# Optimization experiments

Measured on AMD Instinct MI355X. Metric: run time of the kernel, lower is better.

## Reference

```python
import jax, jax.numpy as jnp
import numpy as np

DIM = 64   # flow dimension
HID = 8    # hidden_dim=[8]
B = 131072 # batch of samples


def setup_inputs() -> dict:
    key = jax.random.key(0)
    ks = jax.random.split(key, 6)
    L = DIM - 1  # number of per-dim MLPs (layers[0..L-1], layer l has fan-in l+1)
    lim = float(np.sqrt(0.5))
    x = jax.random.normal(ks[0], (B, DIM), jnp.float32)
    initial_param = jax.random.uniform(ks[1], (2,), jnp.float32, -lim, lim)
    # Ragged Linear(fan_in=l+1, 8) weights stacked into padded [L, HID, L];
    # entries beyond column l are masked to zero in reference().
    fan_in = np.arange(1, DIM).astype(np.float32)          # (L,)
    bnd1 = (1.0 / np.sqrt(fan_in))[:, None, None]          # torch Linear default init bound
    W1 = jax.random.uniform(ks[2], (L, HID, L), jnp.float32, -1.0, 1.0) * bnd1
    b1 = jax.random.uniform(ks[3], (L, HID), jnp.float32, -1.0, 1.0) * bnd1[:, :, 0]
    bnd2 = 1.0 / np.sqrt(HID)
    W2 = jax.random.uniform(ks[4], (L, 2, HID), jnp.float32, -bnd2, bnd2)
    b2 = jax.random.uniform(ks[5], (L, 2), jnp.float32, -bnd2, bnd2)
    return {"x": x, "initial_param": initial_param, "W1": W1, "b1": b1, "W2": W2, "b2": b2}


def reference(x, initial_param, W1, b1, W2, b2):
    B_, D = x.shape
    L = W1.shape[0]  # D - 1
    # mask[l, d] = 1 iff d <= l  ->  layer l sees exactly x[:, :l+1]
    mask = jnp.tril(jnp.ones((L, L), x.dtype))
    W1m = W1 * mask[:, None, :]
    # all dim-1 tiny MLPs fused into two batched contractions
    h = jnp.tanh(jnp.einsum('bd,lhd->blh', x[:, :L], W1m) + b1)   # [B, L, HID]
    out = jnp.einsum('blh,loh->blo', h, W2) + b2                   # [B, L, 2]
    mu0 = jnp.broadcast_to(initial_param[0], (B_, 1)).astype(x.dtype)
    al0 = jnp.broadcast_to(initial_param[1], (B_, 1)).astype(x.dtype)
    mu = jnp.concatenate([mu0, out[:, :, 0]], axis=1)              # [B, D]
    alpha = jnp.concatenate([al0, out[:, :, 1]], axis=1)           # [B, D]
    z = x * jnp.exp(alpha) + mu
    log_det = jnp.sum(alpha, axis=1)
    return z, log_det
```

## Files before the change

kernel.cpp:

```cpp
#include <hip/hip_runtime.h>


#define DIMS 64

typedef __attribute__((ext_vector_type(8))) short short8;
typedef __attribute__((ext_vector_type(4))) float f32x4;
typedef unsigned short ushort_t;
typedef unsigned int uint_t;
typedef unsigned long long ull_t;

__device__ __forceinline__ ushort_t f2bf(float f) {
    uint_t u = __float_as_uint(f);
    u += 0x7FFFu + ((u >> 16) & 1u);
    return (ushort_t)(u >> 16);
}

__global__ void siaf_prep(const float* __restrict__ W1, const float* __restrict__ b1,
                          const float* __restrict__ W2, const float* __restrict__ b2,
                          ushort_t* __restrict__ ws_u) {
    ushort_t* w1b    = ws_u;
    ushort_t* w2full = ws_u + 512 * 64;
    float*    b2f    = (float*)(ws_u + 512 * 64 + 128 * 64);
    int i = blockIdx.x * 256 + threadIdx.x;
    if (i < 512 * 64) {
        int k = i & 63, n = i >> 6, l = n >> 3, h = n & 7;
        float v = 0.0f;
        if (l < 63) {
            if (k < 63 && k <= l) v = W1[(l * 8 + h) * 63 + k];
            else if (k == 63)     v = b1[l * 8 + h];
        }
        w1b[i] = f2bf(v);
    } else if (i < 512 * 64 + 128 * 64) {
        int j = i - 512 * 64;
        int kl = j & 63, r = j >> 6, l = r >> 1, o = r & 1;
        float v = 0.0f;
        if (l < 63 && (kl >> 3) == (l & 7)) v = W2[(l * 2 + o) * 8 + (kl & 7)];
        w2full[j] = f2bf(v);
    } else if (i < 512 * 64 + 128 * 64 + 128) {
        int j = i - (512 * 64 + 128 * 64);
        int l = j >> 1, o = j & 1;
        b2f[j] = (l < 63) ? b2[l * 2 + o] : 0.0f;
    }
}

__device__ __forceinline__ float tanh_fast(float y) {
    float e = __expf(2.0f * y);
    float r = __builtin_amdgcn_rcpf(e + 1.0f);
    return fmaf(-2.0f, r, 1.0f);
}

__global__ __launch_bounds__(256, 4) void siaf_mfma(
        const float* __restrict__ x, const float* __restrict__ ip,
        const ushort_t* __restrict__ ws_u, float* __restrict__ out, int nB) {
    const ushort_t* w1b    = ws_u;
    const ushort_t* w2full = ws_u + 512 * 64;
    const float*    b2f    = (const float*)(ws_u + 512 * 64 + 128 * 64);

    __shared__ float  xz[4][32 * 64];
    __shared__ uint_t hb[4][2][16 * 16];

    const int tid  = threadIdx.x;
    const int wv   = tid >> 6, lane = tid & 63;
    const int s16  = lane & 15, quad = lane >> 4;
    const int sbase = blockIdx.x * 128 + wv * 32;

    float* xzw = xz[wv];

    #pragma unroll
    for (int g = 0; g < 8; ++g) {
        const float4 v = ((const float4*)(x + (size_t)(sbase + 4 * g) * DIMS))[lane];
        const int s_loc = 4 * g + quad;
        const int chunk = (lane & 15) ^ (s_loc & 15);
        *(float4*)(xzw + s_loc * 64 + chunk * 4) = v;
    }

    const float ip0 = ip[0], ip1 = ip[1];

    short8 bfr[2][2];
    float lsum[2] = {0.0f, 0.0f};
    #pragma unroll
    for (int st = 0; st < 2; ++st) {
        const int s_loc = st * 16 + s16;
        #pragma unroll
        for (int kh = 0; kh < 2; ++kh) {
            const int c0 = kh * 8 + quad * 2;
            float4 va = *(const float4*)(xzw + s_loc * 64 + ((c0 ^ s16) & 15) * 4);
            float4 vb = *(const float4*)(xzw + s_loc * 64 + (((c0 + 1) ^ s16) & 15) * 4);
            float f[8] = {va.x, va.y, va.z, va.w, vb.x, vb.y, vb.z, vb.w};
            if (kh == 1 && quad == 3) f[7] = 1.0f;
            short8 t;
            #pragma unroll
            for (int j = 0; j < 8; ++j) t[j] = (short)f2bf(f[j]);
            bfr[st][kh] = t;
        }
    }

    for (int mt = 0; mt < 8; ++mt) {
        const ushort_t* w2p = w2full + (mt * 16 + s16) * 64 + quad * 8;
        f32x4 acc2[2] = {{0.f, 0.f, 0.f, 0.f}, {0.f, 0.f, 0.f, 0.f}};

        #pragma unroll
        for (int t4 = 0; t4 < 4; ++t4) {
            const ushort_t* w1p = w1b + ((mt * 4 + t4) * 16 + s16) * 64 + quad * 8;
            const short8 a0 = *(const short8*)(w1p);
            const short8 a1 = *(const short8*)(w1p + 32);
            #pragma unroll
            for (int st = 0; st < 2; ++st) {
                f32x4 acc = {0.f, 0.f, 0.f, 0.f};
                acc = __builtin_amdgcn_mfma_f32_16x16x32_bf16(a0, bfr[st][0], acc, 0, 0, 0);
                acc = __builtin_amdgcn_mfma_f32_16x16x32_bf16(a1, bfr[st][1], acc, 0, 0, 0);
                const float t0 = tanh_fast(acc[0]), t1 = tanh_fast(acc[1]);
                const float t2 = tanh_fast(acc[2]), t3 = tanh_fast(acc[3]);
                const uint_t p01 = ((uint_t)f2bf(t1) << 16) | f2bf(t0);
                const uint_t p23 = ((uint_t)f2bf(t3) << 16) | f2bf(t2);
                const int idx = (t4 & 1) * 8 + quad * 2;
                const int ph  = (((idx >> 2) ^ (s16 & 3)) << 2) | (idx & 3);
                *(ull_t*)&hb[wv][st][s16 * 16 + ph] = ((ull_t)p23 << 32) | p01;
            }
            if (t4 & 1) {
                const int half = t4 >> 1;
                const short8 ch = *(const short8*)(w2p + half * 32);
                #pragma unroll
                for (int st = 0; st < 2; ++st) {
                    const int ph = (quad ^ (s16 & 3)) << 2;
                    const short8 hfr = *(const short8*)&hb[wv][st][s16 * 16 + ph];
                    acc2[st] = __builtin_amdgcn_mfma_f32_16x16x32_bf16(ch, hfr, acc2[st], 0, 0, 0);
                }
            }
        }

        const int l0 = mt * 8 + quad * 2;
        const float4 b2v = *(const float4*)(b2f + l0 * 2);
        const bool pad = (l0 == 62);
        #pragma unroll
        for (int st = 0; st < 2; ++st) {
            const int s_loc = st * 16 + s16;
            float mu0 = acc2[st][0] + b2v.x, al0 = acc2[st][1] + b2v.y;
            float mu1 = acc2[st][2] + b2v.z, al1 = acc2[st][3] + b2v.w;
            const int d1 = l0 + 1;
            float* p1 = xzw + s_loc * 64 + (((((d1 >> 2) ^ s16) & 15) << 2) | (d1 & 3));
            *p1 = fmaf(*p1, __expf(al0), mu0);
            lsum[st] += al0;
            const float alB = pad ? ip1 : al1;
            const float muB = pad ? ip0 : mu1;
            const int d2 = pad ? 0 : (l0 + 2);
            float* p2 = xzw + s_loc * 64 + (((((d2 >> 2) ^ s16) & 15) << 2) | (d2 & 3));
            *p2 = fmaf(*p2, __expf(alB), muB);
            lsum[st] += alB;
        }
    }

    #pragma unroll
    for (int g = 0; g < 8; ++g) {
        const int s_loc = 4 * g + quad;
        const int chunk = (lane & 15) ^ (s_loc & 15);
        const float4 v = *(const float4*)(xzw + s_loc * 64 + chunk * 4);
        ((float4*)(out + (size_t)(sbase + 4 * g) * DIMS))[lane] = v;
    }

    #pragma unroll
    for (int st = 0; st < 2; ++st) {
        float v = lsum[st];
        int r1 = __builtin_amdgcn_ds_swizzle(__float_as_int(v), 0x401F);
        v += __int_as_float(r1);
        int r2 = __builtin_amdgcn_ds_bpermute((lane ^ 32) << 2, __float_as_int(v));
        v += __int_as_float(r2);
        if (quad == 0)
            out[(size_t)nB * DIMS + sbase + st * 16 + s16] = v;
    }
}

extern "C" void kernel_launch(void* const* d_in, const int* in_sizes, int n_in,
                              void* d_out, int out_size, void* d_ws, size_t ws_size,
                              hipStream_t stream) {
    const float* x  = (const float*)d_in[0];
    const float* ip = (const float*)d_in[1];
    const float* W1 = (const float*)d_in[2];
    const float* b1 = (const float*)d_in[3];
    const float* W2 = (const float*)d_in[4];
    const float* b2 = (const float*)d_in[5];
    ushort_t* ws = (ushort_t*)d_ws;
    float* out = (float*)d_out;

    const int nB = in_sizes[0] / DIMS;
    const int prep_elems = 512 * 64 + 128 * 64 + 128;

    siaf_prep<<<(prep_elems + 255) / 256, 256, 0, stream>>>(W1, b1, W2, b2, ws);
    siaf_mfma<<<nB / 128, 256, 0, stream>>>(x, ip, ws, out, nB);
}
```

Before: 129.5 us.

## Keep tanh hidden activations in registers and skip zero K-halves of layer one

The W1 rows are permuted in the prep kernel so the first MFMA's output layout matches the B-operand layout of the second MFMA. The packed bf16 tanh results then feed the second MFMA straight from registers, removing the LDS round trip through the hb buffer. b1 is now added through the accumulator initialisation instead of a ones column. The W1 and b1 values are pre-scaled by 2/ln2 so tanh can use exp2, packing uses the hardware bf16 convert, and the upper-K MFMAs are skipped for the first four tiles, where masked weights are zero. The launch-bounds occupancy hint is raised from 4 to 5, at the cost of a more intricate row permutation that must stay consistent between the two kernels.

```diff
diff --git a/kernel.cpp b/kernel.cpp
--- a/kernel.cpp
+++ b/kernel.cpp
@@ -5,9 +5,29 @@
 
 typedef __attribute__((ext_vector_type(8))) short short8;
 typedef __attribute__((ext_vector_type(4))) float f32x4;
+typedef __attribute__((ext_vector_type(4))) unsigned int uint4v;
 typedef unsigned short ushort_t;
 typedef unsigned int uint_t;
-typedef unsigned long long ull_t;
+
+#if __has_builtin(__builtin_amdgcn_exp2f)
+#define YSCALE 2.8853900817779268f
+#define EXPY(x) __builtin_amdgcn_exp2f(x)
+#else
+#define YSCALE 2.0f
+#define EXPY(x) __expf(x)
+#endif
+
+__device__ __forceinline__ uint_t pk2bf(float a, float b) {
+#if __has_builtin(__builtin_amdgcn_cvt_pk_bf16_f32)
+    typedef __attribute__((ext_vector_type(2))) __bf16 bf16x2;
+    bf16x2 r = __builtin_amdgcn_cvt_pk_bf16_f32(a, b);
+    return __builtin_bit_cast(uint_t, r);
+#else
+    uint_t ua = __float_as_uint(a); ua += 0x7FFFu + ((ua >> 16) & 1u);
+    uint_t ub = __float_as_uint(b); ub += 0x7FFFu + ((ub >> 16) & 1u);
+    return (ub & 0xFFFF0000u) | (ua >> 16);
+#endif
+}
 
 __device__ __forceinline__ ushort_t f2bf(float f) {
     uint_t u = __float_as_uint(f);
@@ -15,49 +35,60 @@
     return (ushort_t)(u >> 16);
 }
 
+#define W2F_OFF (512 * 64)
+#define FREG_OFF (512 * 64 + 128 * 64)
+#define PREP_N (512 * 64 + 128 * 64 + 512 + 128)
+
+__device__ __forceinline__ int logrow(int p) {
+    int n = p & 15;
+    return (p >> 5) * 32 + (n >> 2) * 8 + ((p >> 4) & 1) * 4 + (n & 3);
+}
+
 __global__ void siaf_prep(const float* __restrict__ W1, const float* __restrict__ b1,
                           const float* __restrict__ W2, const float* __restrict__ b2,
                           ushort_t* __restrict__ ws_u) {
     ushort_t* w1b    = ws_u;
-    ushort_t* w2full = ws_u + 512 * 64;
-    float*    b2f    = (float*)(ws_u + 512 * 64 + 128 * 64);
+    ushort_t* w2full = ws_u + W2F_OFF;
+    float*    fb     = (float*)(ws_u + FREG_OFF);
     int i = blockIdx.x * 256 + threadIdx.x;
     if (i < 512 * 64) {
-        int k = i & 63, n = i >> 6, l = n >> 3, h = n & 7;
+        int k = i & 63, p = i >> 6;
+        int L = logrow(p), l = L >> 3, h = L & 7;
         float v = 0.0f;
-        if (l < 63) {
-            if (k < 63 && k <= l) v = W1[(l * 8 + h) * 63 + k];
-            else if (k == 63)     v = b1[l * 8 + h];
-        }
+        if (l < 63 && k <= l) v = W1[(l * 8 + h) * 63 + k] * YSCALE;
         w1b[i] = f2bf(v);
-    } else if (i < 512 * 64 + 128 * 64) {
-        int j = i - 512 * 64;
+    } else if (i < FREG_OFF) {
+        int j = i - W2F_OFF;
         int kl = j & 63, r = j >> 6, l = r >> 1, o = r & 1;
         float v = 0.0f;
         if (l < 63 && (kl >> 3) == (l & 7)) v = W2[(l * 2 + o) * 8 + (kl & 7)];
         w2full[j] = f2bf(v);
-    } else if (i < 512 * 64 + 128 * 64 + 128) {
-        int j = i - (512 * 64 + 128 * 64);
+    } else if (i < FREG_OFF + 512) {
+        int p = i - FREG_OFF;
+        int L = logrow(p), l = L >> 3, h = L & 7;
+        fb[p] = (l < 63) ? b1[l * 8 + h] * YSCALE : 0.0f;
+    } else if (i < PREP_N) {
+        int j = i - (FREG_OFF + 512);
         int l = j >> 1, o = j & 1;
-        b2f[j] = (l < 63) ? b2[l * 2 + o] : 0.0f;
-    }
-}
-
-__device__ __forceinline__ float tanh_fast(float y) {
-    float e = __expf(2.0f * y);
+        fb[512 + j] = (l < 63) ? b2[l * 2 + o] : 0.0f;
+    }
+}
+
+__device__ __forceinline__ float th(float t) {
+    float e = EXPY(t);
     float r = __builtin_amdgcn_rcpf(e + 1.0f);
     return fmaf(-2.0f, r, 1.0f);
 }
 
-__global__ __launch_bounds__(256, 4) void siaf_mfma(
+__global__ __launch_bounds__(256, 5) void siaf_mfma(
         const float* __restrict__ x, const float* __restrict__ ip,
         const ushort_t* __restrict__ ws_u, float* __restrict__ out, int nB) {
     const ushort_t* w1b    = ws_u;
-    const ushort_t* w2full = ws_u + 512 * 64;
-    const float*    b2f    = (const float*)(ws_u + 512 * 64 + 128 * 64);
-
-    __shared__ float  xz[4][32 * 64];
-    __shared__ uint_t hb[4][2][16 * 16];
+    const ushort_t* w2full = ws_u + W2F_OFF;
+    const float*    b1f    = (const float*)(ws_u + FREG_OFF);
+    const float*    b2f    = b1f + 512;
+
+    __shared__ float xz[4][32 * 64];
 
     const int tid  = threadIdx.x;
     const int wv   = tid >> 6, lane = tid & 63;
@@ -86,12 +117,9 @@
             const int c0 = kh * 8 + quad * 2;
             float4 va = *(const float4*)(xzw + s_loc * 64 + ((c0 ^ s16) & 15) * 4);
             float4 vb = *(const float4*)(xzw + s_loc * 64 + (((c0 + 1) ^ s16) & 15) * 4);
-            float f[8] = {va.x, va.y, va.z, va.w, vb.x, vb.y, vb.z, vb.w};
-            if (kh == 1 && quad == 3) f[7] = 1.0f;
-            short8 t;
-            #pragma unroll
-            for (int j = 0; j < 8; ++j) t[j] = (short)f2bf(f[j]);
-            bfr[st][kh] = t;
+            uint4v u = {pk2bf(va.x, va.y), pk2bf(va.z, va.w),
+                        pk2bf(vb.x, vb.y), pk2bf(vb.z, vb.w)};
+            bfr[st][kh] = __builtin_bit_cast(short8, u);
         }
     }
 
@@ -100,32 +128,34 @@
         f32x4 acc2[2] = {{0.f, 0.f, 0.f, 0.f}, {0.f, 0.f, 0.f, 0.f}};
 
         #pragma unroll
-        for (int t4 = 0; t4 < 4; ++t4) {
-            const ushort_t* w1p = w1b + ((mt * 4 + t4) * 16 + s16) * 64 + quad * 8;
-            const short8 a0 = *(const short8*)(w1p);
-            const short8 a1 = *(const short8*)(w1p + 32);
+        for (int half = 0; half < 2; ++half) {
+            const int p0 = mt * 4 + half * 2;
+            const ushort_t* w1p0 = w1b + (p0 * 16 + s16) * 64 + quad * 8;
+            const ushort_t* w1p1 = w1p0 + 1024;
+            const short8 a00 = *(const short8*)w1p0;
+            const short8 a10 = *(const short8*)w1p1;
+            const float4 bi0 = *(const float4*)(b1f + p0 * 16 + quad * 4);
+            const float4 bi1 = *(const float4*)(b1f + (p0 + 1) * 16 + quad * 4);
+            const short8 c2 = *(const short8*)(w2p + half * 32);
+            short8 a01, a11;
+            if (mt >= 4) {
+                a01 = *(const short8*)(w1p0 + 32);
+                a11 = *(const short8*)(w1p1 + 32);
+            }
             #pragma unroll
             for (int st = 0; st < 2; ++st) {
-                f32x4 acc = {0.f, 0.f, 0.f, 0.f};
-                acc = __builtin_amdgcn_mfma_f32_16x16x32_bf16(a0, bfr[st][0], acc, 0, 0, 0);
-                acc = __builtin_amdgcn_mfma_f32_16x16x32_bf16(a1, bfr[st][1], acc, 0, 0, 0);
-                const float t0 = tanh_fast(acc[0]), t1 = tanh_fast(acc[1]);
-                const float t2 = tanh_fast(acc[2]), t3 = tanh_fast(acc[3]);
-                const uint_t p01 = ((uint_t)f2bf(t1) << 16) | f2bf(t0);
-                const uint_t p23 = ((uint_t)f2bf(t3) << 16) | f2bf(t2);
-                const int idx = (t4 & 1) * 8 + quad * 2;
-                const int ph  = (((idx >> 2) ^ (s16 & 3)) << 2) | (idx & 3);
-                *(ull_t*)&hb[wv][st][s16 * 16 + ph] = ((ull_t)p23 << 32) | p01;
-            }
-            if (t4 & 1) {
-                const int half = t4 >> 1;
-                const short8 ch = *(const short8*)(w2p + half * 32);
-                #pragma unroll
-                for (int st = 0; st < 2; ++st) {
-                    const int ph = (quad ^ (s16 & 3)) << 2;
-                    const short8 hfr = *(const short8*)&hb[wv][st][s16 * 16 + ph];
-                    acc2[st] = __builtin_amdgcn_mfma_f32_16x16x32_bf16(ch, hfr, acc2[st], 0, 0, 0);
+                f32x4 aE = {bi0.x, bi0.y, bi0.z, bi0.w};
+                f32x4 aO = {bi1.x, bi1.y, bi1.z, bi1.w};
+                aE = __builtin_amdgcn_mfma_f32_16x16x32_bf16(a00, bfr[st][0], aE, 0, 0, 0);
+                aO = __builtin_amdgcn_mfma_f32_16x16x32_bf16(a10, bfr[st][0], aO, 0, 0, 0);
+                if (mt >= 4) {
+                    aE = __builtin_amdgcn_mfma_f32_16x16x32_bf16(a01, bfr[st][1], aE, 0, 0, 0);
+                    aO = __builtin_amdgcn_mfma_f32_16x16x32_bf16(a11, bfr[st][1], aO, 0, 0, 0);
                 }
+                uint4v hh = {pk2bf(th(aE[0]), th(aE[1])), pk2bf(th(aE[2]), th(aE[3])),
+                             pk2bf(th(aO[0]), th(aO[1])), pk2bf(th(aO[2]), th(aO[3]))};
+                const short8 hfr = __builtin_bit_cast(short8, hh);
+                acc2[st] = __builtin_amdgcn_mfma_f32_16x16x32_bf16(c2, hfr, acc2[st], 0, 0, 0);
             }
         }
 
@@ -183,8 +213,7 @@
     float* out = (float*)d_out;
 
     const int nB = in_sizes[0] / DIMS;
-    const int prep_elems = 512 * 64 + 128 * 64 + 128;
-
-    siaf_prep<<<(prep_elems + 255) / 256, 256, 0, stream>>>(W1, b1, W2, b2, ws);
+
+    siaf_prep<<<(PREP_N + 255) / 256, 256, 0, stream>>>(W1, b1, W2, b2, ws);
     siaf_mfma<<<nB / 128, 256, 0, stream>>>(x, ip, ws, out, nB);
 }
```

Result: no change. 130.0 us (+0.4%).
